# Kernel tuning notes

Measured on AMD Instinct MI355X. Metric: run time of the kernel, lower is better.

Reference implementation:

```python
import jax, jax.numpy as jnp
import numpy as np

B, S, H, V_SZ = 256, 49, 2048, 10000

def setup_inputs() -> dict:
    key = jax.random.key(0)
    ks = jax.random.split(key, 24)
    sc = 0.02
    inp = {
        'V': jax.random.normal(ks[0], (B, S, H), jnp.float32),
        'v_g': jax.random.normal(ks[1], (B, H), jnp.float32),
        'state': jax.random.normal(ks[2], (2, 1, B, H), jnp.float32),
        'captions': jax.random.randint(ks[3], (B, 16), 0, V_SZ, jnp.int32),
        'time': 1,
        # params (torch Linear convention: W is (out,in), y = x@W.T+b)
        'fc_W': jax.random.normal(ks[4], (H, H), jnp.float32) * sc,
        'fc_b': jnp.zeros((H,), jnp.float32),
        'att_W': jax.random.normal(ks[5], (H, H), jnp.float32) * sc,
        'att_b': jnp.zeros((H,), jnp.float32),
        'emb': jax.random.normal(ks[6], (V_SZ + 1, H), jnp.float32) * sc,
        'ctx_W': jax.random.normal(ks[7], (H, H), jnp.float32) * sc,
        'ctx_b': jnp.zeros((H,), jnp.float32),
        'a2c_W': jax.random.normal(ks[8], (2 * H, H), jnp.float32) * sc,
        'a2c_b': jnp.zeros((2 * H,), jnp.float32),
        'i2h_W': jax.random.normal(ks[9], (5 * H, H), jnp.float32) * sc,
        'i2h_b': jnp.zeros((5 * H,), jnp.float32),
        'h2h_W': jax.random.normal(ks[10], (5 * H, H), jnp.float32) * sc,
        'h2h_b': jnp.zeros((5 * H,), jnp.float32),
        'h2att_W': jax.random.normal(ks[11], (H, H), jnp.float32) * sc,
        'h2att_b': jnp.zeros((H,), jnp.float32),
        'alpha_W': jax.random.normal(ks[12], (1, H), jnp.float32) * sc,
        'alpha_b': jnp.zeros((1,), jnp.float32),
    }
    return inp


def reference(V, v_g, state, fc_W, fc_b, att_W, att_b, emb, ctx_W, ctx_b,
              a2c_W, a2c_b, i2h_W, i2h_b, h2h_W, h2h_b,
              h2att_W, h2att_b, alpha_W, alpha_b, captions, time):
    # fc_embed(v_g): computed by the original module (unused downstream)
    fc_feats = jax.nn.relu(v_g @ fc_W.T + fc_b)
    # att_embed + ctx2att over the 49 spatial locations
    att_feats = jax.nn.relu(jnp.einsum('bsf,hf->bsh', V, att_W) + att_b)   # (B,49,H)
    p_att = jnp.einsum('bsh,ah->bsa', att_feats, ctx_W) + ctx_b            # (B,49,H)
    # word embedding
    it = captions[:, time]
    xt = jax.nn.relu(emb[it])                                              # (B,H)
    if time == 0:
        state = jnp.zeros_like(state)
    h_prev, c_prev = state[0, -1], state[1, -1]                            # (B,H) each
    # Bahdanau attention
    att_h = h_prev @ h2att_W.T + h2att_b                                   # (B,H)
    dot = jnp.tanh(p_att + att_h[:, None, :])                              # (B,49,H)
    scores = jnp.einsum('bsh,h->bs', dot, alpha_W[0]) + alpha_b[0]         # (B,49)
    weight = jax.nn.softmax(scores, axis=1)
    att_res = jnp.einsum('bs,bsh->bh', weight, att_feats)                  # (B,H)
    # LSTM-with-maxout cell
    sums = xt @ i2h_W.T + i2h_b + h_prev @ h2h_W.T + h2h_b                 # (B,5H)
    Hd = h_prev.shape[-1]
    gates = jax.nn.sigmoid(sums[:, :3 * Hd])
    in_gate, forget_gate, out_gate = gates[:, :Hd], gates[:, Hd:2 * Hd], gates[:, 2 * Hd:]
    in_tr = sums[:, 3 * Hd:] + (att_res @ a2c_W.T + a2c_b)                 # (B,2H)
    in_tr = jnp.maximum(in_tr[:, :Hd], in_tr[:, Hd:])                      # maxout
    next_c = forget_gate * c_prev + in_gate * in_tr
    next_h = out_gate * jnp.tanh(next_c)
    output = next_h[:, None, :]                                            # (B,1,H)
    return output, next_h[None], next_c[None]
```

## Files before the change

kernel.cpp:

```cpp
#include <hip/hip_runtime.h>


typedef __bf16 bf16x8 __attribute__((ext_vector_type(8)));
typedef float  f32x4  __attribute__((ext_vector_type(4)));

static constexpr int Bn = 256;
static constexpr int Sn = 49;
static constexpr int Hn = 2048;
static constexpr int Mrows = Bn * Sn;
static constexpr int LDP = 72;

__device__ __forceinline__ unsigned short f2bf(float f) {
    unsigned u = __builtin_bit_cast(unsigned, f);
    u += 0x7FFFu + ((u >> 16) & 1u);
    return (unsigned short)(u >> 16);
}
__device__ __forceinline__ float bf2f(unsigned short h) {
    return __builtin_bit_cast(float, ((unsigned)h) << 16);
}

__global__ void k_convert3(const float* __restrict__ s0, unsigned short* __restrict__ d0, int n0,
                           const float* __restrict__ s1, unsigned short* __restrict__ d1, int n1,
                           const float* __restrict__ s2, unsigned short* __restrict__ d2, int n2) {
    int i = blockIdx.x * blockDim.x + threadIdx.x;
    const float* src; unsigned short* dst;
    if (i < n0)            { src = s0; dst = d0; }
    else if (i < n0 + n1)  { src = s1; dst = d1; i -= n0; }
    else if (i < n0 + n1 + n2) { src = s2; dst = d2; i -= n0 + n1; }
    else return;
    const float4* p = (const float4*)src + (size_t)i * 2;
    float4 a = p[0], b = p[1];
    union { unsigned short us[8]; int4 v; } o;
    o.us[0] = f2bf(a.x); o.us[1] = f2bf(a.y); o.us[2] = f2bf(a.z); o.us[3] = f2bf(a.w);
    o.us[4] = f2bf(b.x); o.us[5] = f2bf(b.y); o.us[6] = f2bf(b.z); o.us[7] = f2bf(b.w);
    ((int4*)dst)[i] = o.v;
}

__global__ void k_gather(const float* __restrict__ emb,
                         const float* __restrict__ state,
                         const int* __restrict__ captions,
                         const int* __restrict__ timep,
                         unsigned short* __restrict__ xt_b,
                         unsigned short* __restrict__ h_b) {
    int b = blockIdx.x;
    int tm = timep[0];
    int it = captions[b * 16 + tm];
    const float* erow = emb + (size_t)it * Hn;
    for (int h = threadIdx.x; h < Hn; h += blockDim.x) {
        float x = erow[h];
        xt_b[(size_t)b * Hn + h] = f2bf(x > 0.f ? x : 0.f);
        float hv = (tm == 0) ? 0.f : state[(size_t)b * Hn + h];
        h_b[(size_t)b * Hn + h] = f2bf(hv);
    }
}

template<int EPI>
__global__ __launch_bounds__(512)
void k_fast2(const unsigned short* __restrict__ A,
             const unsigned short* __restrict__ B,
             const float* __restrict__ bias, void* __restrict__ out,
             const float* __restrict__ atth, const float* __restrict__ alphaW,
             int M, int N, int K) {
    __shared__ __align__(16) unsigned short As[128 * 64];
    __shared__ __align__(16) unsigned short Bs[128 * 64];

    const int tid  = threadIdx.x;
    const int lane = tid & 63;
    const int wave = tid >> 6;

    const int nnt = N >> 7;
    const int cpx = (M >> 7) * nnt >> 3;
    const int T   = (blockIdx.x & 7) * cpx + (blockIdx.x >> 3);
    const int m0 = (T / nnt) * 128;
    const int n0 = (T % nnt) * 128;

    const int wm = (wave >> 2) * 64;
    const int wn = (wave & 3) * 32;

    const int srow = lane >> 3;
    const int scol = ((lane & 7) ^ srow) << 3;

    const int rfrag = lane & 15;
    const int ck0 = (((lane >> 4) << 3)) ^ ((lane & 7) << 3);
    const int ck1 = (32 + ((lane >> 4) << 3)) ^ ((lane & 7) << 3);

    f32x4 acc[4][2];
#pragma unroll
    for (int i = 0; i < 4; ++i)
#pragma unroll
        for (int j = 0; j < 2; ++j)
#pragma unroll
            for (int r = 0; r < 4; ++r) acc[i][j][r] = 0.f;

    for (int kt = 0; kt < K; kt += 64) {
        __syncthreads();
#pragma unroll
        for (int i = 0; i < 2; ++i) {
            const int chunk = wave * 2 + i;
            const int r = chunk * 8 + srow;
            __builtin_amdgcn_global_load_lds(
                (const __attribute__((address_space(1))) void*)(A + (size_t)(m0 + r) * K + kt + scol),
                (__attribute__((address_space(3))) void*)(&As[chunk * 512]), 16, 0, 0);
            __builtin_amdgcn_global_load_lds(
                (const __attribute__((address_space(1))) void*)(B + (size_t)(n0 + r) * K + kt + scol),
                (__attribute__((address_space(3))) void*)(&Bs[chunk * 512]), 16, 0, 0);
        }
        __syncthreads();

#pragma unroll
        for (int ks = 0; ks < 2; ++ks) {
            const int cka = ks ? ck1 : ck0;
            bf16x8 af[4], bfr[2];
#pragma unroll
            for (int i = 0; i < 4; ++i)
                af[i] = *(const bf16x8*)&As[(wm + i * 16 + rfrag) * 64 + cka];
#pragma unroll
            for (int j = 0; j < 2; ++j)
                bfr[j] = *(const bf16x8*)&Bs[(wn + j * 16 + rfrag) * 64 + cka];
#pragma unroll
            for (int i = 0; i < 4; ++i)
#pragma unroll
                for (int j = 0; j < 2; ++j)
                    acc[i][j] = __builtin_amdgcn_mfma_f32_16x16x32_bf16(
                        af[i], bfr[j], acc[i][j], 0, 0, 0);
        }
    }

#pragma unroll
    for (int i = 0; i < 4; ++i) {
#pragma unroll
        for (int r = 0; r < 4; ++r) {
            const int gm = m0 + wm + i * 16 + ((lane >> 4) << 2) + r;
            if constexpr (EPI == 3) {
                float partial = 0.f;
                const int b = gm / Sn;
#pragma unroll
                for (int j = 0; j < 2; ++j) {
                    const int gn = n0 + wn + j * 16 + rfrag;
                    float v = acc[i][j][r] + bias[gn] + atth[(size_t)b * N + gn];
                    partial += tanhf(v) * alphaW[gn];
                }
#pragma unroll
                for (int off = 1; off < 16; off <<= 1)
                    partial += __shfl_xor(partial, off);
                if (rfrag == 0) {
                    const int col = (n0 >> 7) * 4 + (wave & 3);
                    ((float*)out)[(size_t)col * M + gm] = partial;
                }
            } else {
#pragma unroll
                for (int j = 0; j < 2; ++j) {
                    const int gn = n0 + wn + j * 16 + rfrag;
                    float v = acc[i][j][r] + bias[gn];
                    ((unsigned short*)out)[(size_t)gm * N + gn] = f2bf(v > 0.f ? v : 0.f);
                }
            }
        }
    }
}

__global__ void k_scored(const float* __restrict__ sp, float* __restrict__ scores, int M) {
    int i = blockIdx.x * blockDim.x + threadIdx.x;
    if (i >= M) return;
    float s = 0.f;
#pragma unroll
    for (int c = 0; c < 64; ++c) s += sp[(size_t)c * M + i];
    scores[i] = s;
}

__global__ __launch_bounds__(256)
void k_gemm_pre(const unsigned short* __restrict__ xtb,
                const unsigned short* __restrict__ hb,
                const float* __restrict__ i2h_W, const float* __restrict__ h2h_W,
                const float* __restrict__ h2att_W,
                const float* __restrict__ i2h_b, const float* __restrict__ h2h_b,
                const float* __restrict__ h2att_b,
                float* __restrict__ sums, float* __restrict__ atth) {
    __shared__ __align__(16) unsigned short As[128 * LDP];
    __shared__ __align__(16) unsigned short Bs[128 * LDP];

    const int K = Hn;
    const bool isPre = blockIdx.x < 80;
    const int n0 = (isPre ? blockIdx.x : (blockIdx.x - 80)) * 128;
    const int Nld = isPre ? 5 * Hn : Hn;
    float* outp = isPre ? sums : atth;

    const int tid = threadIdx.x;
    const int m0 = blockIdx.y * 128;
    const int lane = tid & 63;
    const int wave = tid >> 6;
    const int wm = (wave >> 1) * 64;
    const int wn = (wave & 1) * 64;

    f32x4 acc[4][4];
#pragma unroll
    for (int i = 0; i < 4; ++i)
#pragma unroll
        for (int j = 0; j < 4; ++j)
#pragma unroll
            for (int r = 0; r < 4; ++r) acc[i][j][r] = 0.f;

    const int npass = isPre ? 2 : 1;
    for (int pass = 0; pass < npass; ++pass) {
        const unsigned short* Ap = pass ? hb : (isPre ? xtb : hb);
        const float* Bp = pass ? h2h_W : (isPre ? i2h_W : h2att_W);
        for (int kt = 0; kt < K; kt += 64) {
            __syncthreads();
            {
                const int r = tid >> 3, c = (tid & 7) << 3;
                const unsigned short* src = Ap + (size_t)(m0 + r) * K + kt + c;
#pragma unroll
                for (int i = 0; i < 4; ++i) {
                    int4 v = *(const int4*)(src + (size_t)i * 32 * K);
                    *(int4*)&As[(r + i * 32) * LDP + c] = v;
                }
            }
            {
                const int r = tid >> 4, c = (tid & 15) << 2;
                const float* src = Bp + (size_t)(n0 + r) * K + kt + c;
#pragma unroll
                for (int i = 0; i < 8; ++i) {
                    float4 v = *(const float4*)(src + (size_t)i * 16 * K);
                    union { unsigned short us[4]; uint2 u2; } t;
                    t.us[0] = f2bf(v.x); t.us[1] = f2bf(v.y);
                    t.us[2] = f2bf(v.z); t.us[3] = f2bf(v.w);
                    *(uint2*)&Bs[(r + i * 16) * LDP + c] = t.u2;
                }
            }
            __syncthreads();
#pragma unroll
            for (int ks = 0; ks < 64; ks += 32) {
                const int col = ks + ((lane >> 4) << 3);
                const int ra = wm + (lane & 15);
                const int rb = wn + (lane & 15);
                bf16x8 af[4], bfr[4];
#pragma unroll
                for (int i = 0; i < 4; ++i)
                    af[i] = *(const bf16x8*)&As[(ra + i * 16) * LDP + col];
#pragma unroll
                for (int j = 0; j < 4; ++j)
                    bfr[j] = *(const bf16x8*)&Bs[(rb + j * 16) * LDP + col];
#pragma unroll
                for (int i = 0; i < 4; ++i)
#pragma unroll
                    for (int j = 0; j < 4; ++j)
                        acc[i][j] = __builtin_amdgcn_mfma_f32_16x16x32_bf16(
                            af[i], bfr[j], acc[i][j], 0, 0, 0);
            }
        }
    }

#pragma unroll
    for (int i = 0; i < 4; ++i) {
#pragma unroll
        for (int r = 0; r < 4; ++r) {
            const int gm = m0 + wm + i * 16 + ((lane >> 4) << 2) + r;
#pragma unroll
            for (int j = 0; j < 4; ++j) {
                const int gn = n0 + wn + j * 16 + (lane & 15);
                float v = acc[i][j][r] +
                          (isPre ? (i2h_b[gn] + h2h_b[gn]) : h2att_b[gn]);
                outp[(size_t)gm * Nld + gn] = v;
            }
        }
    }
}

__global__ __launch_bounds__(256)
void k_gemm_s(const unsigned short* __restrict__ A, const float* __restrict__ B,
              const float* __restrict__ bias,
              float* __restrict__ out, int M, int N, int K) {
    __shared__ __align__(16) unsigned short As[128 * LDP];
    __shared__ __align__(16) unsigned short Bs[128 * LDP];

    const int tid = threadIdx.x;
    const int m0 = blockIdx.y * 128;
    const int n0 = blockIdx.x * 128;
    const int lane = tid & 63;
    const int wave = tid >> 6;
    const int wm = (wave >> 1) * 64;
    const int wn = (wave & 1) * 64;

    f32x4 acc[4][4];
#pragma unroll
    for (int i = 0; i < 4; ++i)
#pragma unroll
        for (int j = 0; j < 4; ++j)
#pragma unroll
            for (int r = 0; r < 4; ++r) acc[i][j][r] = 0.f;

    for (int kt = 0; kt < K; kt += 64) {
        __syncthreads();
        {
            const int r = tid >> 3, c = (tid & 7) << 3;
            const unsigned short* src = A + (size_t)(m0 + r) * K + kt + c;
#pragma unroll
            for (int i = 0; i < 4; ++i) {
                int4 v = *(const int4*)(src + (size_t)i * 32 * K);
                *(int4*)&As[(r + i * 32) * LDP + c] = v;
            }
        }
        {
            const int r = tid >> 4, c = (tid & 15) << 2;
            const float* src = B + (size_t)(n0 + r) * K + kt + c;
#pragma unroll
            for (int i = 0; i < 8; ++i) {
                float4 v = *(const float4*)(src + (size_t)i * 16 * K);
                union { unsigned short us[4]; uint2 u2; } t;
                t.us[0] = f2bf(v.x); t.us[1] = f2bf(v.y);
                t.us[2] = f2bf(v.z); t.us[3] = f2bf(v.w);
                *(uint2*)&Bs[(r + i * 16) * LDP + c] = t.u2;
            }
        }
        __syncthreads();
#pragma unroll
        for (int ks = 0; ks < 64; ks += 32) {
            const int col = ks + ((lane >> 4) << 3);
            const int ra = wm + (lane & 15);
            const int rb = wn + (lane & 15);
            bf16x8 af[4], bfr[4];
#pragma unroll
            for (int i = 0; i < 4; ++i)
                af[i] = *(const bf16x8*)&As[(ra + i * 16) * LDP + col];
#pragma unroll
            for (int j = 0; j < 4; ++j)
                bfr[j] = *(const bf16x8*)&Bs[(rb + j * 16) * LDP + col];
#pragma unroll
            for (int i = 0; i < 4; ++i)
#pragma unroll
                for (int j = 0; j < 4; ++j)
                    acc[i][j] = __builtin_amdgcn_mfma_f32_16x16x32_bf16(
                        af[i], bfr[j], acc[i][j], 0, 0, 0);
        }
    }

#pragma unroll
    for (int i = 0; i < 4; ++i) {
#pragma unroll
        for (int r = 0; r < 4; ++r) {
            const int gm = m0 + wm + i * 16 + ((lane >> 4) << 2) + r;
#pragma unroll
            for (int j = 0; j < 4; ++j) {
                const int gn = n0 + wn + j * 16 + (lane & 15);
                out[(size_t)gm * N + gn] = acc[i][j][r] + bias[gn];
            }
        }
    }
}

__global__ void k_attres_sm(const float* __restrict__ scores,
                            const unsigned short* __restrict__ attf,
                            unsigned short* __restrict__ attres) {
    int b = blockIdx.y;
    int h = blockIdx.x * blockDim.x + threadIdx.x;
    const float* sc = scores + b * Sn;
    float m = -1e30f;
#pragma unroll 7
    for (int s = 0; s < Sn; ++s) m = fmaxf(m, sc[s]);
    float sum = 0.f;
#pragma unroll 7
    for (int s = 0; s < Sn; ++s) sum += __expf(sc[s] - m);
    const float inv = 1.f / sum;
    const unsigned short* p = attf + (size_t)b * Sn * Hn + h;
    float acc = 0.f;
#pragma unroll 7
    for (int s = 0; s < Sn; ++s)
        acc += __expf(sc[s] - m) * bf2f(p[(size_t)s * Hn]);
    attres[(size_t)b * Hn + h] = f2bf(acc * inv);
}

__global__ void k_final(const float* __restrict__ sums, const float* __restrict__ a2c,
                        const float* __restrict__ state, const int* __restrict__ timep,
                        float* __restrict__ out) {
    int idx = blockIdx.x * blockDim.x + threadIdx.x;
    int b = idx >> 11, h = idx & (Hn - 1);
    const float* srow = sums + (size_t)b * 5 * Hn;
    float ig = 1.f / (1.f + __expf(-srow[h]));
    float fg = 1.f / (1.f + __expf(-srow[Hn + h]));
    float og = 1.f / (1.f + __expf(-srow[2 * Hn + h]));
    float t1 = srow[3 * Hn + h] + a2c[(size_t)b * 2 * Hn + h];
    float t2 = srow[4 * Hn + h] + a2c[(size_t)b * 2 * Hn + Hn + h];
    float intr = fmaxf(t1, t2);
    float cprev = (timep[0] == 0) ? 0.f : state[(size_t)Bn * Hn + idx];
    float c = fg * cprev + ig * intr;
    float hh = og * tanhf(c);
    const int BH = Bn * Hn;
    out[idx] = hh;
    out[BH + idx] = hh;
    out[2 * BH + idx] = c;
}

extern "C" void kernel_launch(void* const* d_in, const int* in_sizes, int n_in,
                              void* d_out, int out_size, void* d_ws, size_t ws_size,
                              hipStream_t stream) {
    const float* V        = (const float*)d_in[0];
    const float* state    = (const float*)d_in[2];
    const int*   captions = (const int*)d_in[3];
    const int*   timep    = (const int*)d_in[4];
    const float* att_W    = (const float*)d_in[7];
    const float* att_b    = (const float*)d_in[8];
    const float* emb      = (const float*)d_in[9];
    const float* ctx_W    = (const float*)d_in[10];
    const float* ctx_b    = (const float*)d_in[11];
    const float* a2c_W    = (const float*)d_in[12];
    const float* a2c_b    = (const float*)d_in[13];
    const float* i2h_W    = (const float*)d_in[14];
    const float* i2h_b    = (const float*)d_in[15];
    const float* h2h_W    = (const float*)d_in[16];
    const float* h2h_b    = (const float*)d_in[17];
    const float* h2att_W  = (const float*)d_in[18];
    const float* h2att_b  = (const float*)d_in[19];
    const float* alpha_W  = (const float*)d_in[20];

    unsigned short* Vb      = (unsigned short*)d_ws;
    unsigned short* attWb   = Vb + (size_t)Mrows * Hn;
    unsigned short* ctxWb   = attWb + (size_t)Hn * Hn;
    unsigned short* attfb   = ctxWb + (size_t)Hn * Hn;
    unsigned short* xtb     = attfb + (size_t)Mrows * Hn;
    unsigned short* hb      = xtb + Bn * Hn;
    unsigned short* attresb = hb + Bn * Hn;
    float* atth    = (float*)(attresb + Bn * Hn);
    float* scores  = atth + Bn * Hn;
    float* weight  = scores + Mrows;
    float* sums    = weight + Mrows;
    float* a2c_out = sums + (size_t)Bn * 5 * Hn;
    float* scorep  = (float*)attWb;

    const int nc0 = Mrows * Hn / 8, nc1 = Hn * Hn / 8, nc2 = Hn * Hn / 8;
    k_convert3<<<(nc0 + nc1 + nc2 + 255) / 256, 256, 0, stream>>>(
        V, Vb, nc0, att_W, attWb, nc1, ctx_W, ctxWb, nc2);
    k_gather<<<Bn, 256, 0, stream>>>(emb, state, captions, timep, xtb, hb);

    const int nwg = (Mrows / 128) * (Hn / 128);

    k_fast2<0><<<nwg, 512, 0, stream>>>(
        Vb, attWb, att_b, attfb, nullptr, nullptr, Mrows, Hn, Hn);
    k_gemm_pre<<<dim3(96, 2), 256, 0, stream>>>(
        xtb, hb, i2h_W, h2h_W, h2att_W, i2h_b, h2h_b, h2att_b, sums, atth);
    k_fast2<3><<<nwg, 512, 0, stream>>>(
        attfb, ctxWb, ctx_b, scorep, atth, alpha_W, Mrows, Hn, Hn);
    k_scored<<<(Mrows + 255) / 256, 256, 0, stream>>>(scorep, scores, Mrows);
    k_attres_sm<<<dim3(Hn / 256, Bn), 256, 0, stream>>>(scores, attfb, attresb);
    k_gemm_s<<<dim3(2 * Hn / 128, Bn / 128), 256, 0, stream>>>(
        attresb, a2c_W, a2c_b, a2c_out, Bn, 2 * Hn, Hn);

    k_final<<<Bn * Hn / 256, 256, 0, stream>>>(sums, a2c_out, state, timep, (float*)d_out);
}
```

Before: 529.1 us.

## Double-buffer LDS tiles to overlap global loads with MFMA compute

The bf16 GEMM kernel now uses two LDS buffers for the A and B tiles. It prefetches the next K-tile with global_load_lds while running MFMAs on the current one, and replaces the two barriers per iteration with one vmcnt wait plus a barrier. The goal is to hide global-memory latency behind matrix math in the large attention-projection GEMMs. The cost is double the LDS footprint (64 KB per block), which can lower occupancy. The final iteration also issues a redundant reload of the last tile.

```diff
diff --git a/kernel.cpp b/kernel.cpp
--- a/kernel.cpp
+++ b/kernel.cpp
@@ -61,8 +61,8 @@
              const float* __restrict__ bias, void* __restrict__ out,
              const float* __restrict__ atth, const float* __restrict__ alphaW,
              int M, int N, int K) {
-    __shared__ __align__(16) unsigned short As[128 * 64];
-    __shared__ __align__(16) unsigned short Bs[128 * 64];
+    __shared__ __align__(16) unsigned short As[2][128 * 64];
+    __shared__ __align__(16) unsigned short Bs[2][128 * 64];
 
     const int tid  = threadIdx.x;
     const int lane = tid & 63;
@@ -92,31 +92,40 @@
 #pragma unroll
             for (int r = 0; r < 4; ++r) acc[i][j][r] = 0.f;
 
-    for (int kt = 0; kt < K; kt += 64) {
-        __syncthreads();
-#pragma unroll
-        for (int i = 0; i < 2; ++i) {
-            const int chunk = wave * 2 + i;
-            const int r = chunk * 8 + srow;
-            __builtin_amdgcn_global_load_lds(
-                (const __attribute__((address_space(1))) void*)(A + (size_t)(m0 + r) * K + kt + scol),
-                (__attribute__((address_space(3))) void*)(&As[chunk * 512]), 16, 0, 0);
-            __builtin_amdgcn_global_load_lds(
-                (const __attribute__((address_space(1))) void*)(B + (size_t)(n0 + r) * K + kt + scol),
-                (__attribute__((address_space(3))) void*)(&Bs[chunk * 512]), 16, 0, 0);
-        }
-        __syncthreads();
-
+#define STG2(BUF, KT)                                                        \
+    {                                                                        \
+        _Pragma("unroll")                                                    \
+        for (int i_ = 0; i_ < 2; ++i_) {                                     \
+            const int chunk_ = wave * 2 + i_;                                \
+            const int r_ = chunk_ * 8 + srow;                                \
+            __builtin_amdgcn_global_load_lds(                                \
+                (const __attribute__((address_space(1))) void*)(A + (size_t)(m0 + r_) * K + (KT) + scol), \
+                (__attribute__((address_space(3))) void*)(&As[BUF][chunk_ * 512]), 16, 0, 0); \
+            __builtin_amdgcn_global_load_lds(                                \
+                (const __attribute__((address_space(1))) void*)(B + (size_t)(n0 + r_) * K + (KT) + scol), \
+                (__attribute__((address_space(3))) void*)(&Bs[BUF][chunk_ * 512]), 16, 0, 0); \
+        }                                                                    \
+    }
+
+    STG2(0, 0);
+    __syncthreads();
+
+    const int NKT = K / 64;
+    for (int kti = 0; kti < NKT; ++kti) {
+        const int cur = kti & 1;
+        const int ktn = (kti + 1 < NKT) ? (kti + 1) * 64 : kti * 64;
+        STG2(cur ^ 1, ktn);
+        __builtin_amdgcn_sched_barrier(0);
 #pragma unroll
         for (int ks = 0; ks < 2; ++ks) {
             const int cka = ks ? ck1 : ck0;
             bf16x8 af[4], bfr[2];
 #pragma unroll
             for (int i = 0; i < 4; ++i)
-                af[i] = *(const bf16x8*)&As[(wm + i * 16 + rfrag) * 64 + cka];
+                af[i] = *(const bf16x8*)&As[cur][(wm + i * 16 + rfrag) * 64 + cka];
 #pragma unroll
             for (int j = 0; j < 2; ++j)
-                bfr[j] = *(const bf16x8*)&Bs[(wn + j * 16 + rfrag) * 64 + cka];
+                bfr[j] = *(const bf16x8*)&Bs[cur][(wn + j * 16 + rfrag) * 64 + cka];
 #pragma unroll
             for (int i = 0; i < 4; ++i)
 #pragma unroll
@@ -124,7 +133,10 @@
                     acc[i][j] = __builtin_amdgcn_mfma_f32_16x16x32_bf16(
                         af[i], bfr[j], acc[i][j], 0, 0, 0);
         }
-    }
+        asm volatile("s_waitcnt vmcnt(0)" ::: "memory");
+        __builtin_amdgcn_s_barrier();
+    }
+#undef STG2
 
 #pragma unroll
     for (int i = 0; i < 4; ++i) {
```

New measurement: 558.8 us. 5.6% more time.
